# Optimization experiments

Hardware: AMD Instinct MI355X
Metric: run time of the kernel (lower is better)

The kernel has to match this reference:

```python
import jax, jax.numpy as jnp
import numpy as np

B, N = 4096, 8192
PULSE_LO = 40.0 / 60.0   # Hz
PULSE_HI = 250.0 / 60.0  # Hz


def setup_inputs() -> dict:
    key = jax.random.key(0)
    k1, k2 = jax.random.split(key)
    outputs = jax.random.normal(k1, (B, N), dtype=jnp.float32)
    # reference heart rates in Hz, uniform inside the pulse band
    targets = jax.random.uniform(k2, (B, 1), dtype=jnp.float32,
                                 minval=PULSE_LO, maxval=PULSE_HI)
    return {"outputs": outputs, "targets": targets, "Fs": 20}


def reference(outputs, targets, Fs):
    n = outputs.shape[-1]
    F = n // 2 + 1
    f = jnp.linspace(0.0, Fs / 2.0, F, dtype=jnp.float32)  # [F]

    min_idx = jnp.argmin(jnp.abs(f - PULSE_LO))
    max_idx = jnp.argmin(jnp.abs(f - PULSE_HI))

    # normalized rFFT power spectrum (torch.rfft(..., normalized=True) divides by sqrt(N))
    X = jnp.fft.rfft(outputs) * (1.0 / np.sqrt(n))          # [B, F] complex
    P1 = X.real ** 2 + X.imag ** 2                          # [B, F]

    # per-sample reference bin index
    r = jnp.argmin(jnp.abs(f[None, :] - targets.reshape(-1, 1)), axis=1)  # [B]
    rb = r[:, None]                                         # [B, 1]
    i = jnp.arange(F)[None, :]                              # [1, F]

    # signal mask u: 1 at ref and 1st harmonic, 0.5 at ref+-1 (applied after, as in torch)
    u = jnp.where((i == rb - 1) | (i == rb + 1), 0.5,
                  jnp.where((i == rb) | (i == 2 * rb), 1.0, 0.0))
    # noise mask w = 1 - u, zeroed outside pulse band and around 1st harmonic
    w = jnp.where((i < min_idx) | (i >= max_idx) |
                  (i == 2 * rb - 1) | (i == 2 * rb + 1),
                  0.0, 1.0 - u)

    signal_energy = jnp.sum(P1 * u, axis=1)                 # [B]
    noise_energy = jnp.sum(P1 * w, axis=1)                  # [B]
    losses = -10.0 * jnp.log(signal_energy / (noise_energy + 1.0)) / jnp.log(10.0)
    return jnp.mean(losses)
```

## Files before the change

### kernel.cpp

```cpp
#include <hip/hip_runtime.h>
#include <math.h>

#define TPB 256
#define ROWS 4

typedef float cplx __attribute__((ext_vector_type(2)));

__device__ __forceinline__ cplx cmul(cplx a, cplx b) {
    return a.xx * b + cplx{-a.y, a.y} * b.yx;
}

__device__ __forceinline__ void dft4(cplx& a, cplx& b, cplx& c, cplx& d) {
    cplx t0 = a + c, t1 = a - c, t2 = b + d, t3 = b - d;
    a = t0 + t2;
    c = t0 - t2;
    cplx jt3 = cplx{t3.y, -t3.x};
    b = t1 + jt3;
    d = t1 - jt3;
}

#define T16(j) (4 * ((j) & 3) + ((j) >> 2))

__device__ __forceinline__ void dft16(cplx v[16]) {
#pragma unroll
    for (int j = 0; j < 4; ++j) dft4(v[j], v[4 + j], v[8 + j], v[12 + j]);
    const float C1 = 0.9238795325112867f, S1 = 0.3826834323650898f;
    const float R2 = 0.7071067811865476f;
    v[5]  = cmul(v[5],  cplx{ C1, -S1});
    v[9]  = cmul(v[9],  cplx{ R2, -R2});
    v[13] = cmul(v[13], cplx{ S1, -C1});
    v[6]  = cmul(v[6],  cplx{ R2, -R2});
    v[10] = cplx{v[10].y, -v[10].x};
    v[14] = cmul(v[14], cplx{-R2, -R2});
    v[7]  = cmul(v[7],  cplx{ S1, -C1});
    v[11] = cmul(v[11], cplx{-R2, -R2});
    v[15] = cmul(v[15], cplx{-C1,  S1});
#pragma unroll
    for (int b = 0; b < 4; ++b) dft4(v[4 * b], v[4 * b + 1], v[4 * b + 2], v[4 * b + 3]);
}

__global__ __launch_bounds__(TPB, 2) void snr_kernel(const float* __restrict__ x,
                                                     const float* __restrict__ targets,
                                                     float* __restrict__ out) {
    __shared__ __align__(16) cplx Z[4096];
    float* zf = (float*)Z;

    const int t = threadIdx.x;
    const int tl = t & 15;
    const int rb = t ^ ((t >> 4) & 15);
    const int wb0 = t << 4;
    const int row0 = blockIdx.x * ROWS;

    cplx a[16], pf[16];
    {
        const cplx* rowp = (const cplx*)(x + (size_t)row0 * 8192);
#pragma unroll
        for (int l = 0; l < 16; ++l) a[l] = rowp[t + 256 * l];
    }

    float lossSum = 0.f;

#pragma unroll
    for (int it = 0; it < ROWS; ++it) {
        if (it + 1 < ROWS) {
            const cplx* rowp = (const cplx*)(x + (size_t)(row0 + it + 1) * 8192);
#pragma unroll
            for (int l = 0; l < 16; ++l) pf[l] = rowp[t + 256 * l];
        }

        int r;
        {
            float tg = targets[row0 + it];
            const float df = 0.00244140625f;
            int c0 = (int)(tg * 409.6f) - 2;
            if (c0 < 0) c0 = 0;
            r = c0;
            float best = fabsf(df * (float)c0 - tg);
            for (int i = c0 + 1; i <= c0 + 4 && i <= 4096; ++i) {
                float dd = fabsf(df * (float)i - tg);
                if (dd < best) { best = dd; r = i; }
            }
        }

        dft16(a);
        {
            float ang = -1.5339807878856412e-3f * (float)t;
            float sn, cs; __sincosf(ang, &sn, &cs);
            cplx w1 = cplx{cs, sn};
            cplx w2 = cmul(w1, w1), w3 = cmul(w2, w1);
            cplx w4 = cmul(w2, w2), w8 = cmul(w4, w4), w12 = cmul(w8, w4);
            cplx wa[4] = {cplx{1.f, 0.f}, w1, w2, w3};
            cplx wb[4] = {cplx{1.f, 0.f}, w4, w8, w12};
#pragma unroll
            for (int m = 1; m < 16; ++m) {
                int j = T16(m);
                a[j] = cmul(a[j], cmul(wb[m >> 2], wa[m & 3]));
            }
        }
#pragma unroll
        for (int j = 0; j < 16; ++j) Z[wb0 + (T16(j) ^ tl)] = a[j];
        __syncthreads();

#pragma unroll
        for (int l = 0; l < 16; ++l) a[l] = Z[rb + (l << 8)];
        __syncthreads();
        dft16(a);
        {
            const int p = t >> 4;
            float ang = -0.02454369260617026f * (float)p;
            float sn, cs; __sincosf(ang, &sn, &cs);
            cplx w1 = cplx{cs, sn};
            cplx w2 = cmul(w1, w1), w3 = cmul(w2, w1);
            cplx w4 = cmul(w2, w2), w8 = cmul(w4, w4), w12 = cmul(w8, w4);
            cplx wa[4] = {cplx{1.f, 0.f}, w1, w2, w3};
            cplx wb[4] = {cplx{1.f, 0.f}, w4, w8, w12};
#pragma unroll
            for (int m = 1; m < 16; ++m) {
                int j = T16(m);
                a[j] = cmul(a[j], cmul(wb[m >> 2], wa[m & 3]));
            }
        }
        {
            const int base1 = (t >> 4) << 8;
#pragma unroll
            for (int m = 0; m < 16; ++m) {
                Z[base1 + (m << 4) + (tl ^ m)] = a[T16(m)];
            }
        }
        __syncthreads();

#pragma unroll
        for (int l = 0; l < 16; ++l) a[l] = Z[rb + (l << 8)];
        __syncthreads();
        dft16(a);

#pragma unroll
        for (int j = 0; j < 16; ++j) Z[wb0 + (T16(j) ^ tl)] = a[j];
        __syncthreads();

        float band = 0.f;
        {
            float ang = -7.669903939428206e-4f * (float)t;
            float sn, cs; __sincosf(ang, &sn, &cs);
            cplx wku = cplx{cs, sn};
            const float WCc[7] = {1.f, 0.9807852804032304f, 0.9238795325112867f,
                                  0.8314696123025452f, 0.7071067811865476f,
                                  0.5555702330196022f, 0.3826834323650898f};
            const float WCs[7] = {0.f, -0.19509032201612825f, -0.3826834323650898f,
                                  -0.5555702330196022f, -0.7071067811865476f,
                                  -0.8314696123025452f, -0.9238795325112867f};
            const int pc = ((256 - t) & 255) << 4;
            const int pl = (16 - tl) & 15;
#pragma unroll
            for (int m = 1; m <= 6; ++m) {
                const int k = t + (m << 8);
                const int za = t ? (pc | ((15 - m) ^ pl)) : (16 - m);
                cplx Zk = a[T16(m)];
                cplx Zn = Z[za];
                cplx wk = cmul(wku, cplx{WCc[m], WCs[m]});
                cplx Znc = cplx{Zn.x, -Zn.y};
                cplx s  = Zk + Znc;
                cplx dd = Zk - Znc;
                cplx tt = cmul(wk, dd);
                cplx X  = s + cplx{tt.y, -tt.x};
                float P = (X.x * X.x + X.y * X.y) * (1.0f / 32768.0f);
                if ((unsigned)(k - 273) <= 1433u) band += P;
            }
        }

        float capP = 0.f;
        if (t < 6) {
            const int c = (t < 3) ? (r - 1 + t) : (2 * r - 4 + t);
            const int kk = (c <= 2048) ? c : (4096 - c);
            const int nb = (4096 - kk) & 4095;
            const int zka = ((kk & 255) << 4) | ((kk >> 8) ^ (kk & 15));
            const int zna = ((nb & 255) << 4) | ((nb >> 8) ^ (nb & 15));
            cplx Zk = Z[zka], Zn = Z[zna];
            float ang = -7.669903939428206e-4f * (float)kk;
            float sn, cs; __sincosf(ang, &sn, &cs);
            cplx wk = cplx{cs, sn};
            cplx Znc = cplx{Zn.x, -Zn.y};
            cplx s  = Zk + Znc;
            cplx dd = Zk - Znc;
            cplx tt = cmul(wk, dd);
            cplx X  = (c <= 2048) ? (s + cplx{tt.y, -tt.x})
                                  : (s + cplx{-tt.y, tt.x});
            capP = (X.x * X.x + X.y * X.y) * (1.0f / 32768.0f);
        }
        __syncthreads();

        if (t < 6) zf[t] = capP;

#pragma unroll
        for (int off = 32; off > 0; off >>= 1) band += __shfl_down(band, off);
        if ((t & 63) == 0) zf[8 + (t >> 6)] = band;
        __syncthreads();

        if (t == 0) {
            float bb = zf[8] + zf[9] + zf[10] + zf[11];
            float S = zf[1] + zf[4] + 0.5f * (zf[0] + zf[2]);
            float noise = bb;
            const int r2 = 2 * r;
            if (r <= 1706)      noise -= zf[1];
            if (r - 1 >= 273)   noise -= 0.5f * zf[0];
            if (r + 1 <= 1706)  noise -= 0.5f * zf[2];
            if (r2 - 1 <= 1706) noise -= zf[3];
            if (r2 <= 1706)     noise -= zf[4];
            if (r2 + 1 <= 1706) noise -= zf[5];
            lossSum += -10.0f * log10f(S / (noise + 1.0f));
        }

        if (it + 1 < ROWS) {
#pragma unroll
            for (int l = 0; l < 16; ++l) a[l] = pf[l];
        }
    }

    if (t == 0) atomicAdd(out, lossSum * (1.0f / 4096.0f));
}

extern "C" void kernel_launch(void* const* d_in, const int* in_sizes, int n_in,
                              void* d_out, int out_size, void* d_ws, size_t ws_size,
                              hipStream_t stream) {
    const float* x = (const float*)d_in[0];
    const float* tg = (const float*)d_in[1];
    float* out = (float*)d_out;
    hipMemsetAsync(out, 0, sizeof(float), stream);
    snr_kernel<<<4096 / ROWS, TPB, 0, stream>>>(x, tg, out);
}
```

Before: 204.5 us.

## Prefetch next row via async global-to-LDS DMA and hoist twiddles out of loop

Replaces the register prefetch of the next row with global_load_lds transfers into a dedicated LDS buffer, issued after the first transpose so they overlap the remaining FFT stages. Twiddle factors for both stages and the post-processing are computed once before the row loop and kept in registers. Regular __syncthreads is replaced by a custom barrier that waits only on lgkmcnt, and the row loop is no longer unrolled. This is meant to cut register pressure and redundant sincos work, at the cost of doubling LDS per block, which may reduce occupancy. The custom barrier does not wait on vmcnt, so ordering of the DMA against the next row's reads depends on the final plain __syncthreads.

Result: faster. 198.6 us (-2.9%).

```diff
diff --git a/kernel.cpp b/kernel.cpp
--- a/kernel.cpp
+++ b/kernel.cpp
@@ -5,6 +5,9 @@
 #define ROWS 4
 
 typedef float cplx __attribute__((ext_vector_type(2)));
+
+typedef const __attribute__((address_space(1))) char gchar_t;
+typedef __attribute__((address_space(3))) char lchar_t;
 
 __device__ __forceinline__ cplx cmul(cplx a, cplx b) {
     return a.xx * b + cplx{-a.y, a.y} * b.yx;
@@ -39,34 +42,84 @@
     for (int b = 0; b < 4; ++b) dft4(v[4 * b], v[4 * b + 1], v[4 * b + 2], v[4 * b + 3]);
 }
 
+__device__ __forceinline__ void bar_lds() {
+    asm volatile("s_waitcnt lgkmcnt(0)" ::: "memory");
+    __builtin_amdgcn_s_barrier();
+    asm volatile("" ::: "memory");
+}
+
+__device__ __forceinline__ void dma_row(const float* rowp, char* ldsbase,
+                                        int wid, int lane) {
+    const char* g = (const char*)rowp + wid * 8192 + lane * 16;
+    char* l = ldsbase + wid * 8192;
+#pragma unroll
+    for (int j = 0; j < 8; ++j) {
+        __builtin_amdgcn_global_load_lds((gchar_t*)(g + j * 1024),
+                                         (lchar_t*)(l + j * 1024), 16, 0, 0);
+    }
+}
+
 __global__ __launch_bounds__(TPB, 2) void snr_kernel(const float* __restrict__ x,
                                                      const float* __restrict__ targets,
                                                      float* __restrict__ out) {
-    __shared__ __align__(16) cplx Z[4096];
-    float* zf = (float*)Z;
+    __shared__ __align__(16) cplx A[4096];
+    __shared__ __align__(16) cplx B[4096];
+    float* zf = (float*)B;
 
     const int t = threadIdx.x;
     const int tl = t & 15;
     const int rb = t ^ ((t >> 4) & 15);
-    const int wb0 = t << 4;
+    const int wbase = t << 4;
     const int row0 = blockIdx.x * ROWS;
-
-    cplx a[16], pf[16];
+    const int wid = t >> 6, lane = t & 63;
+
+    cplx tw0[16], tw1[16], wkb[7];
     {
-        const cplx* rowp = (const cplx*)(x + (size_t)row0 * 8192);
-#pragma unroll
-        for (int l = 0; l < 16; ++l) a[l] = rowp[t + 256 * l];
-    }
+        float ang = -1.5339807878856412e-3f * (float)t;
+        float sn, cs; __sincosf(ang, &sn, &cs);
+        cplx w1 = cplx{cs, sn};
+        cplx u2 = cmul(w1, w1), u3 = cmul(u2, w1);
+        cplx v4 = cmul(u2, u2), v8 = cmul(v4, v4), v12 = cmul(v8, v4);
+        cplx ua[4] = {cplx{1.f, 0.f}, w1, u2, u3};
+        cplx vb[4] = {cplx{1.f, 0.f}, v4, v8, v12};
+#pragma unroll
+        for (int m = 0; m < 16; ++m) tw0[m] = cmul(vb[m >> 2], ua[m & 3]);
+    }
+    {
+        float ang = -0.02454369260617026f * (float)(t >> 4);
+        float sn, cs; __sincosf(ang, &sn, &cs);
+        cplx w1 = cplx{cs, sn};
+        cplx u2 = cmul(w1, w1), u3 = cmul(u2, w1);
+        cplx v4 = cmul(u2, u2), v8 = cmul(v4, v4), v12 = cmul(v8, v4);
+        cplx ua[4] = {cplx{1.f, 0.f}, w1, u2, u3};
+        cplx vb[4] = {cplx{1.f, 0.f}, v4, v8, v12};
+#pragma unroll
+        for (int m = 0; m < 16; ++m) tw1[m] = cmul(vb[m >> 2], ua[m & 3]);
+    }
+    {
+        float ang = -7.669903939428206e-4f * (float)t;
+        float sn, cs; __sincosf(ang, &sn, &cs);
+        cplx wku = cplx{cs, sn};
+        const float WCc[7] = {1.f, 0.9807852804032304f, 0.9238795325112867f,
+                              0.8314696123025452f, 0.7071067811865476f,
+                              0.5555702330196022f, 0.3826834323650898f};
+        const float WCs[7] = {0.f, -0.19509032201612825f, -0.3826834323650898f,
+                              -0.5555702330196022f, -0.7071067811865476f,
+                              -0.8314696123025452f, -0.9238795325112867f};
+#pragma unroll
+        for (int m = 1; m <= 6; ++m) wkb[m] = cmul(wku, cplx{WCc[m], WCs[m]});
+    }
+
+    dma_row(x + (size_t)row0 * 8192, (char*)A, wid, lane);
+    __syncthreads();
 
     float lossSum = 0.f;
 
-#pragma unroll
+#pragma unroll 1
     for (int it = 0; it < ROWS; ++it) {
-        if (it + 1 < ROWS) {
-            const cplx* rowp = (const cplx*)(x + (size_t)(row0 + it + 1) * 8192);
-#pragma unroll
-            for (int l = 0; l < 16; ++l) pf[l] = rowp[t + 256 * l];
-        }
+        cplx a[16];
+#pragma unroll
+        for (int l = 0; l < 16; ++l) a[l] = A[t + 256 * l];
 
         int r;
         {
@@ -83,72 +136,38 @@
         }
 
         dft16(a);
-        {
-            float ang = -1.5339807878856412e-3f * (float)t;
-            float sn, cs; __sincosf(ang, &sn, &cs);
-            cplx w1 = cplx{cs, sn};
-            cplx w2 = cmul(w1, w1), w3 = cmul(w2, w1);
-            cplx w4 = cmul(w2, w2), w8 = cmul(w4, w4), w12 = cmul(w8, w4);
-            cplx wa[4] = {cplx{1.f, 0.f}, w1, w2, w3};
-            cplx wb[4] = {cplx{1.f, 0.f}, w4, w8, w12};
-#pragma unroll
-            for (int m = 1; m < 16; ++m) {
-                int j = T16(m);
-                a[j] = cmul(a[j], cmul(wb[m >> 2], wa[m & 3]));
-            }
-        }
-#pragma unroll
-        for (int j = 0; j < 16; ++j) Z[wb0 + (T16(j) ^ tl)] = a[j];
-        __syncthreads();
-
-#pragma unroll
-        for (int l = 0; l < 16; ++l) a[l] = Z[rb + (l << 8)];
-        __syncthreads();
+#pragma unroll
+        for (int m = 1; m < 16; ++m) { int j = T16(m); a[j] = cmul(a[j], tw0[m]); }
+#pragma unroll
+        for (int j = 0; j < 16; ++j) B[wbase + (T16(j) ^ tl)] = a[j];
+        bar_lds();
+
+        if (it + 1 < ROWS) dma_row(x + (size_t)(row0 + it + 1) * 8192, (char*)A, wid, lane);
+
+#pragma unroll
+        for (int l = 0; l < 16; ++l) a[l] = B[rb + (l << 8)];
+        bar_lds();
         dft16(a);
-        {
-            const int p = t >> 4;
-            float ang = -0.02454369260617026f * (float)p;
-            float sn, cs; __sincosf(ang, &sn, &cs);
-            cplx w1 = cplx{cs, sn};
-            cplx w2 = cmul(w1, w1), w3 = cmul(w2, w1);
-            cplx w4 = cmul(w2, w2), w8 = cmul(w4, w4), w12 = cmul(w8, w4);
-            cplx wa[4] = {cplx{1.f, 0.f}, w1, w2, w3};
-            cplx wb[4] = {cplx{1.f, 0.f}, w4, w8, w12};
-#pragma unroll
-            for (int m = 1; m < 16; ++m) {
-                int j = T16(m);
-                a[j] = cmul(a[j], cmul(wb[m >> 2], wa[m & 3]));
-            }
-        }
+#pragma unroll
+        for (int m = 1; m < 16; ++m) { int j = T16(m); a[j] = cmul(a[j], tw1[m]); }
         {
             const int base1 = (t >> 4) << 8;
 #pragma unroll
-            for (int m = 0; m < 16; ++m) {
-                Z[base1 + (m << 4) + (tl ^ m)] = a[T16(m)];
-            }
-        }
-        __syncthreads();
-
-#pragma unroll
-        for (int l = 0; l < 16; ++l) a[l] = Z[rb + (l << 8)];
-        __syncthreads();
+            for (int m = 0; m < 16; ++m) B[base1 + (m << 4) + (tl ^ m)] = a[T16(m)];
+        }
+        bar_lds();
+
+#pragma unroll
+        for (int l = 0; l < 16; ++l) a[l] = B[rb + (l << 8)];
+        bar_lds();
         dft16(a);
 
 #pragma unroll
-        for (int j = 0; j < 16; ++j) Z[wb0 + (T16(j) ^ tl)] = a[j];
-        __syncthreads();
+        for (int j = 0; j < 16; ++j) B[wbase + (T16(j) ^ tl)] = a[j];
+        bar_lds();
 
         float band = 0.f;
         {
-            float ang = -7.669903939428206e-4f * (float)t;
-            float sn, cs; __sincosf(ang, &sn, &cs);
-            cplx wku = cplx{cs, sn};
-            const float WCc[7] = {1.f, 0.9807852804032304f, 0.9238795325112867f,
-                                  0.8314696123025452f, 0.7071067811865476f,
-                                  0.5555702330196022f, 0.3826834323650898f};
-            const float WCs[7] = {0.f, -0.19509032201612825f, -0.3826834323650898f,
-                                  -0.5555702330196022f, -0.7071067811865476f,
-                                  -0.8314696123025452f, -0.9238795325112867f};
             const int pc = ((256 - t) & 255) << 4;
             const int pl = (16 - tl) & 15;
 #pragma unroll
@@ -156,12 +175,11 @@
                 const int k = t + (m << 8);
                 const int za = t ? (pc | ((15 - m) ^ pl)) : (16 - m);
                 cplx Zk = a[T16(m)];
-                cplx Zn = Z[za];
-                cplx wk = cmul(wku, cplx{WCc[m], WCs[m]});
+                cplx Zn = B[za];
                 cplx Znc = cplx{Zn.x, -Zn.y};
                 cplx s  = Zk + Znc;
                 cplx dd = Zk - Znc;
-                cplx tt = cmul(wk, dd);
+                cplx tt = cmul(wkb[m], dd);
                 cplx X  = s + cplx{tt.y, -tt.x};
                 float P = (X.x * X.x + X.y * X.y) * (1.0f / 32768.0f);
                 if ((unsigned)(k - 273) <= 1433u) band += P;
@@ -175,7 +193,7 @@
             const int nb = (4096 - kk) & 4095;
             const int zka = ((kk & 255) << 4) | ((kk >> 8) ^ (kk & 15));
             const int zna = ((nb & 255) << 4) | ((nb >> 8) ^ (nb & 15));
-            cplx Zk = Z[zka], Zn = Z[zna];
+            cplx Zk = B[zka], Zn = B[zna];
             float ang = -7.669903939428206e-4f * (float)kk;
             float sn, cs; __sincosf(ang, &sn, &cs);
             cplx wk = cplx{cs, sn};
@@ -187,13 +205,14 @@
                                   : (s + cplx{-tt.y, tt.x});
             capP = (X.x * X.x + X.y * X.y) * (1.0f / 32768.0f);
         }
-        __syncthreads();
+        bar_lds();
 
         if (t < 6) zf[t] = capP;
 
 #pragma unroll
         for (int off = 32; off > 0; off >>= 1) band += __shfl_down(band, off);
         if ((t & 63) == 0) zf[8 + (t >> 6)] = band;
+
         __syncthreads();
 
         if (t == 0) {
@@ -209,11 +228,6 @@
             if (r2 + 1 <= 1706) noise -= zf[5];
             lossSum += -10.0f * log10f(S / (noise + 1.0f));
         }
-
-        if (it + 1 < ROWS) {
-#pragma unroll
-            for (int l = 0; l < 16; ++l) a[l] = pf[l];
-        }
     }
 
     if (t == 0) atomicAdd(out, lossSum * (1.0f / 4096.0f));
```
